# Kernel optimization log

Measured on AMD Instinct MI355X. Metric: run time of the kernel, lower is better.

The kernel has to match this reference:

```python
import jax, jax.numpy as jnp
import numpy as np


def _log_g(x):
    # log of g(x) = where(x>=0, x+0.5, sigmoid(x)), computed stably in log space
    return jnp.where(x >= 0.0, jnp.log(jax.nn.relu(x) + 0.5), -jax.nn.softplus(-x))


def setup_inputs() -> dict:
    key = jax.random.key(0)
    k1, k2, k3, k4 = jax.random.split(key, 4)
    B, T, D, H = 4, 8192, 512, 512
    x = jax.random.normal(k1, (B, T, D), dtype=jnp.float32)
    h_prev = jax.random.uniform(k2, (B, 1, H), dtype=jnp.float32)  # positive: log(h0) taken
    W_h = jax.random.normal(k3, (H, D), dtype=jnp.float32) * (1.0 / np.sqrt(D))
    b_h = jnp.zeros((H,), dtype=jnp.float32)
    W_z = jax.random.normal(k4, (H, D), dtype=jnp.float32) * (1.0 / np.sqrt(D))
    b_z = jnp.zeros((H,), dtype=jnp.float32)
    return {"x": x, "h_prev": h_prev, "W_h": W_h, "b_h": b_h, "W_z": W_z, "b_z": b_z}


def reference(x, h_prev, W_h, b_h, W_z, b_z):
    # parallel (seq_len > 1) minGRU forward via Heinsen log-space scan
    k = jnp.einsum('btd,hd->bth', x, W_z) + b_z           # (B,T,H) gate pre-activation
    log_z = -jax.nn.softplus(-k)                          # log sigmoid(k)
    log_coeffs = -jax.nn.softplus(k)                      # log (1 - sigmoid(k))
    log_tilde_h = _log_g(jnp.einsum('btd,hd->bth', x, W_h) + b_h)
    log_h0 = jnp.log(h_prev)                              # (B,1,H)
    log_values = jnp.concatenate([log_h0, log_z + log_tilde_h], axis=1)  # (B,T+1,H)
    # a_star = [0, cumsum(log_coeffs)]
    a_star = jnp.pad(jnp.cumsum(log_coeffs, axis=1), ((0, 0), (1, 0), (0, 0)))
    log_h = a_star + jax.lax.cumlogsumexp(log_values - a_star, axis=1)
    h = jnp.exp(log_h)[:, 1:]                             # drop h0 -> (B,T,H)
    return h
```

## Files before the change

kernel.cpp:

```cpp
#include <hip/hip_runtime.h>
#include <hip/hip_bf16.h>
#include <stdint.h>

#define B_ 4
#define T_ 8192
#define D_ 512
#define H_ 512
#define M_ (B_ * T_)
#define SEG 32
#define SPB 256
#define NSEG (M_ / SEG)

typedef __attribute__((ext_vector_type(8))) short short8;
typedef __attribute__((ext_vector_type(4))) float floatx4;
typedef __attribute__((ext_vector_type(2))) unsigned int uint2e;
typedef __attribute__((ext_vector_type(2))) float float2e;

__device__ __forceinline__ unsigned short f2bf(float f) {
    union { float f; unsigned int u; } v; v.f = f;
    unsigned int u = v.u;
    u += 0x7fffu + ((u >> 16) & 1u);
    return (unsigned short)(u >> 16);
}
__device__ __forceinline__ float bf_lo(unsigned int u) {
    union { unsigned int i; float f; } a; a.i = u << 16; return a.f;
}
__device__ __forceinline__ float bf_hi(unsigned int u) {
    union { unsigned int i; float f; } a; a.i = u & 0xffff0000u; return a.f;
}
__device__ __forceinline__ unsigned int pk_cd(float c, float d) {
    return (unsigned int)f2bf(c) | ((unsigned int)f2bf(d) << 16);
}

__global__ void conv_all(const float* __restrict__ x,
                         const float* __restrict__ Wz,
                         const float* __restrict__ Wh,
                         unsigned short* __restrict__ xbf,
                         unsigned short* __restrict__ Wf)
{
    const int X4 = M_ * D_ / 4;
    const int W4 = H_ * D_ / 4;
    int i = blockIdx.x * blockDim.x + threadIdx.x;
    const float* src; unsigned short* dst; int idx;
    if (i < X4)             { src = x;  dst = xbf;                  idx = i; }
    else if (i < X4 + W4)   { src = Wz; dst = Wf;                   idx = i - X4; }
    else if (i < X4 + 2*W4) { src = Wh; dst = Wf + (size_t)H_ * D_; idx = i - X4 - W4; }
    else return;
    float4 v = ((const float4*)src)[idx];
    ushort4 w; w.x = f2bf(v.x); w.y = f2bf(v.y); w.z = f2bf(v.z); w.w = f2bf(v.w);
    ((ushort4*)dst)[idx] = w;
}

#define LDSB 35840

__global__ __launch_bounds__(256, 3)
void gemm_cd(const unsigned short* __restrict__ xbf,
             const unsigned short* __restrict__ Wf,
             const float* __restrict__ bz, const float* __restrict__ bh,
             unsigned int* __restrict__ cd,
             float2* __restrict__ Sagg)
{
    __shared__ __align__(16) char smem[LDSB];
    unsigned short* lds = (unsigned short*)smem;
    unsigned int*   cdl = (unsigned int*)smem;

    const int tid  = threadIdx.x;
    const int lane = tid & 63;
    const int wave = tid >> 6;
    const int xcd  = blockIdx.x & 7;
    const int nblk = (blockIdx.x >> 3) & 7;
    const int mblk = xcd * 32 + (blockIdx.x >> 6);
    const int m0 = mblk * 128;
    const int n0 = nblk * 64;
    const int wm = (wave >> 1) * 64;
    const int wn = (wave & 1) * 32;
    const int l15  = lane & 15;
    const int quad = lane >> 4;
    const int srow = lane >> 2;
    const int sp   = lane & 3;

    #define STAGE(p, kt)                                                          \
    {                                                                             \
        const int kb = (kt) * 32;                                                 \
        unsigned short* bb = lds + (p) * 8192;                                    \
        _Pragma("unroll")                                                         \
        for (int r = 0; r < 2; ++r) {                                             \
            const int chunk = r * 4 + wave;                                       \
            const int row   = chunk * 16 + srow;                                  \
            const int kp    = sp ^ (row & 3);                                     \
            __builtin_amdgcn_global_load_lds(                                     \
                (const __attribute__((address_space(1))) unsigned int*)           \
                    (xbf + (size_t)(m0 + row) * D_ + kb + kp * 8),                \
                (__attribute__((address_space(3))) unsigned int*)(bb + chunk * 512),\
                16, 0, 0);                                                        \
        }                                                                         \
        {                                                                         \
            const int row = wave * 16 + srow;                                     \
            const int kp  = sp ^ (row & 3);                                       \
            __builtin_amdgcn_global_load_lds(                                     \
                (const __attribute__((address_space(1))) unsigned int*)           \
                    (Wf + (size_t)(n0 + row) * D_ + kb + kp * 8),                 \
                (__attribute__((address_space(3))) unsigned int*)(bb + 4096 + wave * 512),\
                16, 0, 0);                                                        \
            __builtin_amdgcn_global_load_lds(                                     \
                (const __attribute__((address_space(1))) unsigned int*)           \
                    (Wf + (size_t)(512 + n0 + row) * D_ + kb + kp * 8),           \
                (__attribute__((address_space(3))) unsigned int*)(bb + 6144 + wave * 512),\
                16, 0, 0);                                                        \
        }                                                                         \
    }

    floatx4 acc_z[4][2], acc_h[4][2];
    #pragma unroll
    for (int i = 0; i < 4; ++i)
        #pragma unroll
        for (int j = 0; j < 2; ++j) { acc_z[i][j] = (floatx4)0.0f; acc_h[i][j] = (floatx4)0.0f; }

    STAGE(0, 0);

    for (int kt = 0; kt < 16; ++kt) {
        __syncthreads();
        const int base = (kt & 1) * 8192;
        short8 af[4], zf[2], hf[2];
        #pragma unroll
        for (int i = 0; i < 4; ++i) {
            const int ra = wm + i * 16 + l15;
            af[i] = *(const short8*)&lds[base + ra * 32 + ((quad ^ (ra & 3)) * 8)];
        }
        #pragma unroll
        for (int j = 0; j < 2; ++j) {
            const int rb = wn + j * 16 + l15;
            zf[j] = *(const short8*)&lds[base + 4096 + rb * 32 + ((quad ^ (rb & 3)) * 8)];
            hf[j] = *(const short8*)&lds[base + 6144 + rb * 32 + ((quad ^ (rb & 3)) * 8)];
        }
        if (kt < 15) STAGE((kt + 1) & 1, kt + 1);
        #pragma unroll
        for (int i = 0; i < 4; ++i)
            #pragma unroll
            for (int j = 0; j < 2; ++j) {
                acc_z[i][j] = __builtin_amdgcn_mfma_f32_16x16x32_bf16(zf[j], af[i], acc_z[i][j], 0, 0, 0);
                acc_h[i][j] = __builtin_amdgcn_mfma_f32_16x16x32_bf16(hf[j], af[i], acc_h[i][j], 0, 0, 0);
            }
    }

    __syncthreads();

    #pragma unroll
    for (int j = 0; j < 2; ++j) {
        const int hlb = wn + j * 16 + quad * 4;
        const float4 bzv = *(const float4*)&bz[n0 + hlb];
        const float4 bhv = *(const float4*)&bh[n0 + hlb];
        #pragma unroll
        for (int i = 0; i < 4; ++i) {
            const int mloc = wm + i * 16 + l15;
            uint4 w;
            #pragma unroll
            for (int r = 0; r < 4; ++r) {
                float kz = acc_z[i][j][r] + ((const float*)&bzv)[r];
                float hp = acc_h[i][j][r] + ((const float*)&bhv)[r];
                float c  = 1.0f / (1.0f + __expf(kz));
                float g  = (hp >= 0.0f) ? (hp + 0.5f) : (1.0f / (1.0f + __expf(-hp)));
                float d  = (1.0f - c) * g;
                ((unsigned int*)&w)[r] = pk_cd(c, d);
            }
            *(uint4*)&cd[(size_t)(m0 + mloc) * H_ + n0 + hlb] = w;
            *(uint4*)&cdl[mloc * 68 + hlb] = w;
        }
    }

    __syncthreads();

    {
        float C = 1.0f, Dv = 0.0f;
        const int t0 = wave * 32;
        #pragma unroll
        for (int t = 0; t < 32; ++t) {
            unsigned int u = cdl[(t0 + t) * 68 + lane];
            float c = bf_lo(u), d = bf_hi(u);
            Dv = fmaf(c, Dv, d);
            C *= c;
        }
        const int chain = (m0 >> 13) * 512 + n0 + lane;
        const int seg   = ((m0 >> 5) & 255) + wave;
        Sagg[(size_t)chain * SPB + seg] = make_float2(C, Dv);
    }
    #undef STAGE
}

__global__ __launch_bounds__(256)
void interseg(const float* __restrict__ h_prev,
              const float2* __restrict__ Sagg,
              float* __restrict__ Hseg)
{
    const int chain = blockIdx.x * 4 + (threadIdx.x >> 6);
    const int lane  = threadIdx.x & 63;
    const float2* spp = Sagg + (size_t)chain * SPB + lane * 4;
    float4 q0 = *(const float4*)&spp[0];
    float4 q1 = *(const float4*)&spp[2];
    float C = q0.x, D = q0.y;
    D = fmaf(q0.z, D, q0.w);  C *= q0.z;
    D = fmaf(q1.x, D, q1.y);  C *= q1.x;
    D = fmaf(q1.z, D, q1.w);  C *= q1.z;
    #pragma unroll
    for (int off = 1; off < 64; off <<= 1) {
        float Cp = __shfl_up(C, off, 64);
        float Dp = __shfl_up(D, off, 64);
        if (lane >= off) { D = fmaf(C, Dp, D); C *= Cp; }
    }
    float Ce = __shfl_up(C, 1, 64);
    float De = __shfl_up(D, 1, 64);
    if (lane == 0) { Ce = 1.0f; De = 0.0f; }
    const float h0 = h_prev[chain];
    float hs = fmaf(Ce, h0, De);
    float4 o;
    o.x = hs;
    hs = fmaf(q0.x, hs, q0.y); o.y = hs;
    hs = fmaf(q0.z, hs, q0.w); o.z = hs;
    hs = fmaf(q1.x, hs, q1.y); o.w = hs;
    *(float4*)&Hseg[(size_t)chain * SPB + lane * 4] = o;
}

__global__ __launch_bounds__(256)
void apply_scan(const unsigned int* __restrict__ cd,
                const float* __restrict__ Hseg,
                float* __restrict__ out)
{
    const int sg = blockIdx.x;
    const int b  = sg >> 8;
    const int s  = sg & 255;
    const int h  = threadIdx.x * 2;
    float hs0 = Hseg[(size_t)(b * 512 + h)     * SPB + s];
    float hs1 = Hseg[(size_t)(b * 512 + h + 1) * SPB + s];
    const unsigned int* base = cd + (size_t)sg * SEG * H_ + h;
    float* ob = out + (size_t)sg * SEG * H_ + h;
    #pragma unroll
    for (int t = 0; t < SEG; ++t) {
        uint2e v = __builtin_nontemporal_load((const uint2e*)(base + (size_t)t * H_));
        hs0 = fmaf(bf_lo(v.x), hs0, bf_hi(v.x));
        hs1 = fmaf(bf_lo(v.y), hs1, bf_hi(v.y));
        float2e o; o.x = hs0; o.y = hs1;
        __builtin_nontemporal_store(o, (float2e*)(ob + (size_t)t * H_));
    }
}

extern "C" void kernel_launch(void* const* d_in, const int* in_sizes, int n_in,
                              void* d_out, int out_size, void* d_ws, size_t ws_size,
                              hipStream_t stream)
{
    const float* x      = (const float*)d_in[0];
    const float* h_prev = (const float*)d_in[1];
    const float* W_h    = (const float*)d_in[2];
    const float* b_h    = (const float*)d_in[3];
    const float* W_z    = (const float*)d_in[4];
    const float* b_z    = (const float*)d_in[5];
    float* out = (float*)d_out;

    unsigned short* xbf = (unsigned short*)d_out;

    char* ws = (char*)d_ws;
    unsigned int* cd = (unsigned int*)ws;
    size_t cd_bytes = (size_t)M_ * H_ * 4;
    unsigned short* Wf = (unsigned short*)(ws + cd_bytes);
    size_t wf_bytes = (size_t)2 * H_ * D_ * sizeof(unsigned short);
    float2* Sagg = (float2*)(ws + cd_bytes + wf_bytes);
    float*  Hseg = (float*)((char*)Sagg + (size_t)2048 * SPB * sizeof(float2));

    {
        int total = M_ * D_ / 4 + 2 * (H_ * D_ / 4);
        conv_all<<<dim3((total + 255) / 256), dim3(256), 0, stream>>>(x, W_z, W_h, xbf, Wf);
    }
    gemm_cd<<<dim3((M_ / 128) * (H_ / 64)), dim3(256), 0, stream>>>(
        xbf, Wf, b_z, b_h, cd, Sagg);
    interseg<<<dim3(512), dim3(256), 0, stream>>>(h_prev, Sagg, Hseg);
    apply_scan<<<dim3(NSEG), dim3(256), 0, stream>>>(cd, Hseg, out);
}
```

Baseline: 194.0 us.

## Fuse x bf16 conversion into GEMM staging and widen apply_scan vectors

Removes the separate pass that converted x to bf16. The GEMM now loads fp32 x straight into registers, converts and packs it to bf16, and writes the swizzled LDS tile after the MFMAs, so the register loads overlap compute. This drops a full write and re-read of the bf16 x buffer. It adds register pressure and VALU conversion work inside the GEMM, and the 8 output-column blocks now each re-read fp32 x at twice the bytes. Separately, apply_scan handles 4 columns per thread with 128-bit loads and stores, and two segments per block.

Result: slower. 210.7 us (+8.6%).

```diff
diff --git a/kernel.cpp b/kernel.cpp
--- a/kernel.cpp
+++ b/kernel.cpp
@@ -13,8 +13,6 @@
 
 typedef __attribute__((ext_vector_type(8))) short short8;
 typedef __attribute__((ext_vector_type(4))) float floatx4;
-typedef __attribute__((ext_vector_type(2))) unsigned int uint2e;
-typedef __attribute__((ext_vector_type(2))) float float2e;
 
 __device__ __forceinline__ unsigned short f2bf(float f) {
     union { float f; unsigned int u; } v; v.f = f;
@@ -32,20 +30,16 @@
     return (unsigned int)f2bf(c) | ((unsigned int)f2bf(d) << 16);
 }
 
-__global__ void conv_all(const float* __restrict__ x,
-                         const float* __restrict__ Wz,
-                         const float* __restrict__ Wh,
-                         unsigned short* __restrict__ xbf,
-                         unsigned short* __restrict__ Wf)
-{
-    const int X4 = M_ * D_ / 4;
+__global__ void conv_w(const float* __restrict__ Wz,
+                       const float* __restrict__ Wh,
+                       unsigned short* __restrict__ Wf)
+{
     const int W4 = H_ * D_ / 4;
     int i = blockIdx.x * blockDim.x + threadIdx.x;
+    if (i >= 2 * W4) return;
     const float* src; unsigned short* dst; int idx;
-    if (i < X4)             { src = x;  dst = xbf;                  idx = i; }
-    else if (i < X4 + W4)   { src = Wz; dst = Wf;                   idx = i - X4; }
-    else if (i < X4 + 2*W4) { src = Wh; dst = Wf + (size_t)H_ * D_; idx = i - X4 - W4; }
-    else return;
+    if (i < W4) { src = Wz; dst = Wf;                  idx = i; }
+    else        { src = Wh; dst = Wf + (size_t)H_ * D_; idx = i - W4; }
     float4 v = ((const float4*)src)[idx];
     ushort4 w; w.x = f2bf(v.x); w.y = f2bf(v.y); w.z = f2bf(v.z); w.w = f2bf(v.w);
     ((ushort4*)dst)[idx] = w;
@@ -54,7 +48,7 @@
 #define LDSB 35840
 
 __global__ __launch_bounds__(256, 3)
-void gemm_cd(const unsigned short* __restrict__ xbf,
+void gemm_cd(const float* __restrict__ x,
              const unsigned short* __restrict__ Wf,
              const float* __restrict__ bz, const float* __restrict__ bh,
              unsigned int* __restrict__ cd,
@@ -78,36 +72,50 @@
     const int quad = lane >> 4;
     const int srow = lane >> 2;
     const int sp   = lane & 3;
-
-    #define STAGE(p, kt)                                                          \
+    const int sxor = sp ^ (srow & 3);
+
+    #define STAGE_W(p, kt)                                                        \
     {                                                                             \
         const int kb = (kt) * 32;                                                 \
         unsigned short* bb = lds + (p) * 8192;                                    \
+        const int row = wave * 16 + srow;                                         \
+        const int kp  = sp ^ (row & 3);                                           \
+        __builtin_amdgcn_global_load_lds(                                         \
+            (const __attribute__((address_space(1))) unsigned int*)               \
+                (Wf + (size_t)(n0 + row) * D_ + kb + kp * 8),                     \
+            (__attribute__((address_space(3))) unsigned int*)(bb + 4096 + wave * 512),\
+            16, 0, 0);                                                            \
+        __builtin_amdgcn_global_load_lds(                                         \
+            (const __attribute__((address_space(1))) unsigned int*)               \
+                (Wf + (size_t)(512 + n0 + row) * D_ + kb + kp * 8),               \
+            (__attribute__((address_space(3))) unsigned int*)(bb + 6144 + wave * 512),\
+            16, 0, 0);                                                            \
+    }
+
+    float4 xr[2][2];
+    #define LOAD_X(kt)                                                            \
+    {                                                                             \
+        _Pragma("unroll")                                                         \
+        for (int r = 0; r < 2; ++r) {                                             \
+            const int row = (r * 4 + wave) * 16 + srow;                           \
+            const float* gp = x + (size_t)(m0 + row) * D_ + (kt) * 32 + sp * 8;   \
+            xr[r][0] = *(const float4*)gp;                                        \
+            xr[r][1] = *(const float4*)(gp + 4);                                  \
+        }                                                                         \
+    }
+    #define WRITE_X(p)                                                            \
+    {                                                                             \
         _Pragma("unroll")                                                         \
         for (int r = 0; r < 2; ++r) {                                             \
             const int chunk = r * 4 + wave;                                       \
-            const int row   = chunk * 16 + srow;                                  \
-            const int kp    = sp ^ (row & 3);                                     \
-            __builtin_amdgcn_global_load_lds(                                     \
-                (const __attribute__((address_space(1))) unsigned int*)           \
-                    (xbf + (size_t)(m0 + row) * D_ + kb + kp * 8),                \
-                (__attribute__((address_space(3))) unsigned int*)(bb + chunk * 512),\
-                16, 0, 0);                                                        \
+            unsigned short* dp = lds + (p) * 8192 + chunk * 512 + srow * 32 + sxor * 8;\
+            uint4 w;                                                              \
+            w.x = pk_cd(xr[r][0].x, xr[r][0].y);                                  \
+            w.y = pk_cd(xr[r][0].z, xr[r][0].w);                                  \
+            w.z = pk_cd(xr[r][1].x, xr[r][1].y);                                  \
+            w.w = pk_cd(xr[r][1].z, xr[r][1].w);                                  \
+            *(uint4*)dp = w;                                                      \
         }                                                                         \
-        {                                                                         \
-            const int row = wave * 16 + srow;                                     \
-            const int kp  = sp ^ (row & 3);                                       \
-            __builtin_amdgcn_global_load_lds(                                     \
-                (const __attribute__((address_space(1))) unsigned int*)           \
-                    (Wf + (size_t)(n0 + row) * D_ + kb + kp * 8),                 \
-                (__attribute__((address_space(3))) unsigned int*)(bb + 4096 + wave * 512),\
-                16, 0, 0);                                                        \
-            __builtin_amdgcn_global_load_lds(                                     \
-                (const __attribute__((address_space(1))) unsigned int*)           \
-                    (Wf + (size_t)(512 + n0 + row) * D_ + kb + kp * 8),           \
-                (__attribute__((address_space(3))) unsigned int*)(bb + 6144 + wave * 512),\
-                16, 0, 0);                                                        \
-        }                                                                         \
     }
 
     floatx4 acc_z[4][2], acc_h[4][2];
@@ -116,7 +124,9 @@
         #pragma unroll
         for (int j = 0; j < 2; ++j) { acc_z[i][j] = (floatx4)0.0f; acc_h[i][j] = (floatx4)0.0f; }
 
-    STAGE(0, 0);
+    LOAD_X(0);
+    STAGE_W(0, 0);
+    WRITE_X(0);
 
     for (int kt = 0; kt < 16; ++kt) {
         __syncthreads();
@@ -133,7 +143,7 @@
             zf[j] = *(const short8*)&lds[base + 4096 + rb * 32 + ((quad ^ (rb & 3)) * 8)];
             hf[j] = *(const short8*)&lds[base + 6144 + rb * 32 + ((quad ^ (rb & 3)) * 8)];
         }
-        if (kt < 15) STAGE((kt + 1) & 1, kt + 1);
+        if (kt < 15) { LOAD_X(kt + 1); STAGE_W((kt + 1) & 1, kt + 1); }
         #pragma unroll
         for (int i = 0; i < 4; ++i)
             #pragma unroll
@@ -141,6 +151,7 @@
                 acc_z[i][j] = __builtin_amdgcn_mfma_f32_16x16x32_bf16(zf[j], af[i], acc_z[i][j], 0, 0, 0);
                 acc_h[i][j] = __builtin_amdgcn_mfma_f32_16x16x32_bf16(hf[j], af[i], acc_h[i][j], 0, 0, 0);
             }
+        if (kt < 15) WRITE_X((kt + 1) & 1);
     }
 
     __syncthreads();
@@ -184,7 +195,9 @@
         const int seg   = ((m0 >> 5) & 255) + wave;
         Sagg[(size_t)chain * SPB + seg] = make_float2(C, Dv);
     }
-    #undef STAGE
+    #undef STAGE_W
+    #undef LOAD_X
+    #undef WRITE_X
 }
 
 __global__ __launch_bounds__(256)
@@ -225,21 +238,25 @@
                 const float* __restrict__ Hseg,
                 float* __restrict__ out)
 {
-    const int sg = blockIdx.x;
+    const int sg = blockIdx.x * 2 + (threadIdx.x >> 7);
     const int b  = sg >> 8;
     const int s  = sg & 255;
-    const int h  = threadIdx.x * 2;
+    const int h  = (threadIdx.x & 127) * 4;
     float hs0 = Hseg[(size_t)(b * 512 + h)     * SPB + s];
     float hs1 = Hseg[(size_t)(b * 512 + h + 1) * SPB + s];
+    float hs2 = Hseg[(size_t)(b * 512 + h + 2) * SPB + s];
+    float hs3 = Hseg[(size_t)(b * 512 + h + 3) * SPB + s];
     const unsigned int* base = cd + (size_t)sg * SEG * H_ + h;
     float* ob = out + (size_t)sg * SEG * H_ + h;
     #pragma unroll
     for (int t = 0; t < SEG; ++t) {
-        uint2e v = __builtin_nontemporal_load((const uint2e*)(base + (size_t)t * H_));
+        uint4 v = *(const uint4*)(base + (size_t)t * H_);
         hs0 = fmaf(bf_lo(v.x), hs0, bf_hi(v.x));
         hs1 = fmaf(bf_lo(v.y), hs1, bf_hi(v.y));
-        float2e o; o.x = hs0; o.y = hs1;
-        __builtin_nontemporal_store(o, (float2e*)(ob + (size_t)t * H_));
+        hs2 = fmaf(bf_lo(v.z), hs2, bf_hi(v.z));
+        hs3 = fmaf(bf_lo(v.w), hs3, bf_hi(v.w));
+        floatx4 o; o[0] = hs0; o[1] = hs1; o[2] = hs2; o[3] = hs3;
+        __builtin_nontemporal_store(o, (floatx4*)(ob + (size_t)t * H_));
     }
 }
 
@@ -255,8 +272,6 @@
     const float* b_z    = (const float*)d_in[5];
     float* out = (float*)d_out;
 
-    unsigned short* xbf = (unsigned short*)d_out;
-
     char* ws = (char*)d_ws;
     unsigned int* cd = (unsigned int*)ws;
     size_t cd_bytes = (size_t)M_ * H_ * 4;
@@ -265,12 +280,9 @@
     float2* Sagg = (float2*)(ws + cd_bytes + wf_bytes);
     float*  Hseg = (float*)((char*)Sagg + (size_t)2048 * SPB * sizeof(float2));
 
-    {
-        int total = M_ * D_ / 4 + 2 * (H_ * D_ / 4);
-        conv_all<<<dim3((total + 255) / 256), dim3(256), 0, stream>>>(x, W_z, W_h, xbf, Wf);
-    }
+    conv_w<<<dim3(512), dim3(256), 0, stream>>>(W_z, W_h, Wf);
     gemm_cd<<<dim3((M_ / 128) * (H_ / 64)), dim3(256), 0, stream>>>(
-        xbf, Wf, b_z, b_h, cd, Sagg);
+        x, Wf, b_z, b_h, cd, Sagg);
     interseg<<<dim3(512), dim3(256), 0, stream>>>(h_prev, Sagg, Hseg);
-    apply_scan<<<dim3(NSEG), dim3(256), 0, stream>>>(cd, Hseg, out);
-}
+    apply_scan<<<dim3(NSEG / 2), dim3(256), 0, stream>>>(cd, Hseg, out);
+}
```
